# Performance work log

Hardware: AMD Instinct MI355X
Metric: run time of the kernel (lower is better)

## Reference

```python
import jax, jax.numpy as jnp
import numpy as np

K = 1024          # num_codebook_vectors
D = 256           # latent_dim
BETA = 0.25
DECAY = 0.99
EPS = 1e-5


def setup_inputs() -> dict:
    key = jax.random.key(0)
    k1, k2, k3 = jax.random.split(key, 3)
    return {
        "z": jax.random.normal(k1, (32, 256, 32, 32), dtype=jnp.float32),
        "embedding": jax.random.normal(k2, (K, D), dtype=jnp.float32),
        "ema_cluster_size": jnp.zeros((K,), dtype=jnp.float32),
        "ema_w": jax.random.normal(k3, (K, D), dtype=jnp.float32),
    }


def reference(z, embedding, ema_cluster_size, ema_w):
    # z: [B, C=D, H, W] -> [B, H, W, D]
    zp = jnp.transpose(z, (0, 2, 3, 1))
    zf = zp.reshape(-1, D)                                  # [N, D]

    # pairwise squared distances: ||z||^2 + ||e||^2 - 2 z e^T
    d = (jnp.sum(zf * zf, axis=1, keepdims=True)
         + jnp.sum(embedding * embedding, axis=1)
         - 2.0 * zf @ embedding.T)                           # [N, K]
    idx = jnp.argmin(d, axis=1)                              # [N]

    # one-hot @ embedding == gather
    z_q = jnp.take(embedding, idx, axis=0).reshape(zp.shape)  # [B,H,W,D]

    # EMA codebook update (training path)
    counts = jax.ops.segment_sum(jnp.ones_like(idx, dtype=jnp.float32), idx,
                                 num_segments=K)             # sum of one-hots
    new_cs = ema_cluster_size * DECAY + (1.0 - DECAY) * counts
    n = jnp.sum(new_cs)
    new_cs = (new_cs + EPS) / (n + K * EPS) * n
    dw = jax.ops.segment_sum(zf, idx, num_segments=K)        # encodings^T @ zf
    new_ema_w = ema_w * DECAY + (1.0 - DECAY) * dw
    new_embedding = new_ema_w / new_cs[:, None]

    # commitment loss (z_q computed with OLD embedding, per source order)
    e_latent_loss = jnp.mean((z_q - zp) ** 2)
    loss = BETA * e_latent_loss

    # straight-through (no grad distinction in pure forward)
    z_q_out = jnp.transpose(z_q, (0, 3, 1, 2))               # [B, D, H, W]
    return (z_q_out, idx[:, None], loss, new_embedding, new_cs, new_ema_w)
```

## Files before the change

kernel.cpp:

```cpp
#include <hip/hip_runtime.h>

#define K_CODES 1024
#define D_DIM   256
#define N_VEC   32768
#define BETA    0.25f
#define DECAY   0.99f
#define EPSV    1e-5f

#define OFF_ZQ   0
#define OFF_IDX  8388608
#define OFF_LOSS 8421376
#define OFF_EMB  8421377
#define OFF_CS   8683521
#define OFF_EMAW 8684545

#define WS_EMBT    0
#define WS_ENORM   262144
#define WS_ELOMAX  263168
#define WS_EHIMAX  263169
#define WS_FIXCNT  263170
#define WS_S2      263172
#define WS_ZN2     1311748
#define WS_ZLO2    1344516
#define WS_FIXLIST 1377284
#define WS_OFF     1410052
#define WS_POS     1411076
#define WS_CNT     1412100
#define WS_CHTAB   1413124
#define WS_TC      1415172

#define CHUNK 32

typedef _Float16 f16;
typedef f16   f16x8 __attribute__((ext_vector_type(8)));
typedef float f32x4 __attribute__((ext_vector_type(4)));

__device__ inline void top2_merge(float& d1, int& j1, float& d2, int& j2,
                                  float od1, int oj1, float od2, int oj2) {
    if (od1 < d1 || (od1 == d1 && oj1 < j1)) {
        float nd2; int nj2;
        if (d1 < od2 || (d1 == od2 && j1 < oj2)) { nd2 = d1; nj2 = j1; }
        else { nd2 = od2; nj2 = oj2; }
        d2 = nd2; j2 = nj2; d1 = od1; j1 = oj1;
    } else {
        if (od1 < d2 || (od1 == d2 && oj1 < j2)) { d2 = od1; j2 = oj1; }
    }
}

__global__ void k_pt(const float* __restrict__ z, const float* __restrict__ emb,
                     float* __restrict__ ws, float* __restrict__ out) {
    if (blockIdx.x == 0 && threadIdx.x == 0) *(int*)(ws + WS_FIXCNT) = 0;
    if (blockIdx.x < 256) {
        int j    = blockIdx.x * 4 + (threadIdx.x >> 6);
        int lane = threadIdx.x & 63;
        float4 v = reinterpret_cast<const float4*>(emb + j * D_DIM)[lane];
        ws[(lane * 4 + 0) * 1024 + j] = v.x;
        ws[(lane * 4 + 1) * 1024 + j] = v.y;
        ws[(lane * 4 + 2) * 1024 + j] = v.z;
        ws[(lane * 4 + 3) * 1024 + j] = v.w;
        float s = v.x * v.x + v.y * v.y + v.z * v.z + v.w * v.w;
        float hx = (float)(f16)v.x, hy = (float)(f16)v.y;
        float hz = (float)(f16)v.z, hw = (float)(f16)v.w;
        float lx = v.x - hx, ly = v.y - hy, lz = v.z - hz, lw = v.w - hw;
        float sl = lx * lx + ly * ly + lz * lz + lw * lw;
        float sh = hx * hx + hy * hy + hz * hz + hw * hw;
        #pragma unroll
        for (int o = 32; o > 0; o >>= 1) {
            s  += __shfl_xor(s,  o, 64);
            sl += __shfl_xor(sl, o, 64);
            sh += __shfl_xor(sh, o, 64);
        }
        if (lane == 0) {
            ws[WS_ENORM + j] = s;
            atomicMax((int*)(ws + WS_ELOMAX), __float_as_int(sqrtf(sl)));
            atomicMax((int*)(ws + WS_EHIMAX), __float_as_int(sqrtf(sh)));
        }
    } else if (blockIdx.x < 384) {
        int slot = (blockIdx.x - 256) * 256 + threadIdx.x;
        int lane = slot & 63;
        int kbjt = slot >> 6;
        int kb   = kbjt & 7;
        int jt   = kbjt >> 3;
        int j    = jt * 16 + (lane & 15);
        int d0   = kb * 32 + (lane >> 4) * 8;
        float4 e0 = *reinterpret_cast<const float4*>(emb + j * D_DIM + d0);
        float4 e1 = *reinterpret_cast<const float4*>(emb + j * D_DIM + d0 + 4);
        f16x8 w;
        w[0] = (f16)e0.x; w[1] = (f16)e0.y; w[2] = (f16)e0.z; w[3] = (f16)e0.w;
        w[4] = (f16)e1.x; w[5] = (f16)e1.y; w[6] = (f16)e1.z; w[7] = (f16)e1.w;
        f16* dst = (f16*)(out + OFF_EMAW + 3);
        *reinterpret_cast<f16x8*>(dst + slot * 8) = w;
    } else {
        __shared__ float tile[32][257];
        const int bid = blockIdx.x - 384;
        const int n0  = bid * 32;
        const int b   = n0 >> 10;
        const int hw0 = n0 & 1023;
        const int tid = threadIdx.x;
        #pragma unroll 8
        for (int rep = 0; rep < 32; ++rep) {
            int elem = rep * 256 + tid;
            int d = elem >> 5, hwl = elem & 31;
            tile[hwl][d] = z[b * (D_DIM * 1024) + d * 1024 + hw0 + hwl];
        }
        __syncthreads();
        #pragma unroll 8
        for (int row = 0; row < 32; ++row)
            out[OFF_ZQ + (long)(n0 + row) * 256 + tid] = tile[row][tid];
        if (tid < 32) {
            float sn = 0.f, sl = 0.f;
            for (int d = 0; d < 256; ++d) {
                float v  = tile[tid][d];
                float lo = v - (float)(f16)v;
                sn += v * v; sl += lo * lo;
            }
            ws[WS_ZN2  + n0 + tid] = sn;
            ws[WS_ZLO2 + n0 + tid] = sl;
        }
    }
}

__global__ __launch_bounds__(256, 4)
void k_main(float* __restrict__ out, float* __restrict__ ws) {
    __shared__ float els_s[512];

    const int tid  = threadIdx.x;
    const int lane = tid & 63;
    const int w    = tid >> 6;
    const int bid  = blockIdx.x;
    const int rt   = bid >> 1;
    const int jh   = bid & 1;
    const int n0   = rt * 64;
    const float* zf = out + OFF_ZQ;
    const f16* Bw = (const f16*)(out + OFF_EMAW + 3);

    if (bid == 0) {
        #pragma unroll
        for (int r = 0; r < 4; ++r) out[OFF_CS + r * 256 + tid] = 0.f;
        if (tid == 0) out[OFF_LOSS] = 0.f;
    }
    els_s[tid]       = ws[WS_ENORM + jh * 512 + tid];
    els_s[tid + 256] = ws[WS_ENORM + jh * 512 + tid + 256];

    const int aoff = (lane >> 4) * 8;
    const int c    = lane & 15;
    const long arow = n0 + w * 16 + c;
    f16x8 a0, a1, a2, a3, a4, a5, a6, a7;
#define LOADA(KB, AV) { \
    float4 p0 = *reinterpret_cast<const float4*>(zf + arow * 256 + KB * 32 + aoff); \
    float4 p1 = *reinterpret_cast<const float4*>(zf + arow * 256 + KB * 32 + aoff + 4); \
    AV = (f16x8){(f16)p0.x, (f16)p0.y, (f16)p0.z, (f16)p0.w, \
                 (f16)p1.x, (f16)p1.y, (f16)p1.z, (f16)p1.w}; }
    LOADA(0, a0) LOADA(1, a1) LOADA(2, a2) LOADA(3, a3)
    LOADA(4, a4) LOADA(5, a5) LOADA(6, a6) LOADA(7, a7)
#undef LOADA
    __syncthreads();

    float d1_0 = 3.4e38f, d2_0 = 3.4e38f; int j1_0 = 0, j2_0 = 0;
    float d1_1 = 3.4e38f, d2_1 = 3.4e38f; int j1_1 = 0, j2_1 = 0;
    float d1_2 = 3.4e38f, d2_2 = 3.4e38f; int j1_2 = 0, j2_2 = 0;
    float d1_3 = 3.4e38f, d2_3 = 3.4e38f; int j1_3 = 0, j2_3 = 0;

    for (int pass = 0; pass < 16; ++pass) {
        const int jt0 = jh * 32 + pass * 2;
        const f16* B0 = Bw + ((size_t)jt0 * 8 * 64 + lane) * 8;
        f32x4 acc0 = (f32x4){0.f, 0.f, 0.f, 0.f};
        f32x4 acc1 = (f32x4){0.f, 0.f, 0.f, 0.f};
#define KBSTEP(KB, AV) { \
        f16x8 b0 = *reinterpret_cast<const f16x8*>(B0 + (size_t)KB * 512); \
        f16x8 b1 = *reinterpret_cast<const f16x8*>(B0 + (size_t)(KB + 8) * 512); \
        acc0 = __builtin_amdgcn_mfma_f32_16x16x32_f16(AV, b0, acc0, 0, 0, 0); \
        acc1 = __builtin_amdgcn_mfma_f32_16x16x32_f16(AV, b1, acc1, 0, 0, 0); }
        KBSTEP(0, a0) KBSTEP(1, a1) KBSTEP(2, a2) KBSTEP(3, a3)
        KBSTEP(4, a4) KBSTEP(5, a5) KBSTEP(6, a6) KBSTEP(7, a7)
#undef KBSTEP
        const int jl0 = pass * 32 + c;
        const float en0 = els_s[jl0];
        const float en1 = els_s[jl0 + 16];
        const int jg0 = jh * 512 + jl0;
#define FOLD(V, JJ, R) { float _v = (V); \
        if (_v < d1_##R) { d2_##R = d1_##R; j2_##R = j1_##R; d1_##R = _v; j1_##R = (JJ); } \
        else if (_v < d2_##R) { d2_##R = _v; j2_##R = (JJ); } }
        FOLD(en0 - 2.f * acc0[0], jg0,      0) FOLD(en1 - 2.f * acc1[0], jg0 + 16, 0)
        FOLD(en0 - 2.f * acc0[1], jg0,      1) FOLD(en1 - 2.f * acc1[1], jg0 + 16, 1)
        FOLD(en0 - 2.f * acc0[2], jg0,      2) FOLD(en1 - 2.f * acc1[2], jg0 + 16, 2)
        FOLD(en0 - 2.f * acc0[3], jg0,      3) FOLD(en1 - 2.f * acc1[3], jg0 + 16, 3)
#undef FOLD
    }

#define MERGE(R, RIDX) { \
        float e1 = d1_##R, e2 = d2_##R; int f1 = j1_##R, f2 = j2_##R; \
        _Pragma("unroll") \
        for (int s = 1; s < 16; s <<= 1) { \
            float o1 = __shfl_xor(e1, s, 64); int g1 = __shfl_xor(f1, s, 64); \
            float o2 = __shfl_xor(e2, s, 64); int g2 = __shfl_xor(f2, s, 64); \
            top2_merge(e1, f1, e2, f2, o1, g1, o2, g2); \
        } \
        if (c == 0) { \
            int row = n0 + w * 16 + (lane >> 4) * 4 + RIDX; \
            *reinterpret_cast<float4*>(ws + WS_S2 + ((size_t)row * 2 + jh) * 4) = \
                (float4){e1, (float)f1, e2, (float)f2}; } }
    MERGE(0, 0) MERGE(1, 1) MERGE(2, 2) MERGE(3, 3)
#undef MERGE
}

__global__ void k_merge(float* __restrict__ ws, float* __restrict__ out) {
    int n = blockIdx.x * 256 + threadIdx.x;
    const float4* S2 = reinterpret_cast<const float4*>(ws + WS_S2) + (size_t)n * 2;
    float4 e0 = S2[0], e1 = S2[1];
    float d1 = e0.x; int j1 = (int)e0.y; float d2 = e0.z; int j2 = (int)e0.w;
    top2_merge(d1, j1, d2, j2, e1.x, (int)e1.y, e1.z, (int)e1.w);
    out[OFF_IDX + n] = (float)j1;
    float zn2 = ws[WS_ZN2 + n];
    float margin = 4.f * (sqrtf(ws[WS_ZLO2 + n]) * ws[WS_EHIMAX] +
                          sqrtf(zn2) * ws[WS_ELOMAX]) + 0.05f;
    if (d2 - d1 <= margin) {
        int p = atomicAdd((int*)(ws + WS_FIXCNT), 1);
        ((int*)(ws + WS_FIXLIST))[p] = n;
    } else {
        atomicAdd(out + OFF_CS + j1, 1.0f);
        atomicAdd(out + OFF_LOSS, d1 + zn2);
    }
    #pragma unroll
    for (int r = 0; r < 2; ++r)
        *reinterpret_cast<float4*>(out + OFF_EMAW + ((size_t)n * 2 + r) * 4) =
            (float4){0.f, 0.f, 0.f, 0.f};
}

__global__ void k_fix(const float* __restrict__ ws_c, float* __restrict__ out) {
    __shared__ float zr[8][256];
    __shared__ float rd[8][4]; __shared__ int rj[8][4];
    const int tid = threadIdx.x;
    const int cnt = *(const int*)(ws_c + WS_FIXCNT);
    const int* fixlist = (const int*)(ws_c + WS_FIXLIST);
    const int groups = (cnt + 7) >> 3;
    const float4 en = *reinterpret_cast<const float4*>(ws_c + WS_ENORM + tid * 4);

    for (int g = blockIdx.x; g < groups; g += gridDim.x) {
        int nrow[8];
        #pragma unroll
        for (int r = 0; r < 8; ++r) {
            int slot = g * 8 + r;
            nrow[r] = (slot < cnt) ? fixlist[slot] : -1;
        }
        #pragma unroll
        for (int r = 0; r < 8; ++r)
            zr[r][tid] = (nrow[r] >= 0) ? out[OFF_ZQ + (long)nrow[r] * 256 + tid] : 0.f;
        __syncthreads();

        float acc[8][4];
        #pragma unroll
        for (int r = 0; r < 8; ++r)
            #pragma unroll
            for (int q = 0; q < 4; ++q) acc[r][q] = 0.f;
        #pragma unroll 4
        for (int d = 0; d < 256; ++d) {
            float4 e = *reinterpret_cast<const float4*>(ws_c + WS_EMBT + d * 1024 + tid * 4);
            #pragma unroll
            for (int r = 0; r < 8; ++r) {
                float zd = zr[r][d];
                acc[r][0] += zd * e.x; acc[r][1] += zd * e.y;
                acc[r][2] += zd * e.z; acc[r][3] += zd * e.w;
            }
        }
        #pragma unroll
        for (int r = 0; r < 8; ++r) {
            float best = 3.4e38f; int bj = 0;
            #pragma unroll
            for (int q = 0; q < 4; ++q) {
                int j = tid * 4 + q;
                float v = ((const float*)&en)[q] - 2.f * acc[r][q];
                if (v < best || (v == best && j < bj)) { best = v; bj = j; }
            }
            #pragma unroll
            for (int o = 1; o < 64; o <<= 1) {
                float ov = __shfl_xor(best, o, 64);
                int   oj = __shfl_xor(bj, o, 64);
                if (ov < best || (ov == best && oj < bj)) { best = ov; bj = oj; }
            }
            if ((tid & 63) == 0) { rd[r][tid >> 6] = best; rj[r][tid >> 6] = bj; }
        }
        __syncthreads();
        if (tid < 8) {
            int r = tid;
            float v = rd[r][0]; int j = rj[r][0];
            #pragma unroll
            for (int ww = 1; ww < 4; ++ww)
                if (rd[r][ww] < v || (rd[r][ww] == v && rj[r][ww] < j)) { v = rd[r][ww]; j = rj[r][ww]; }
            int slot = g * 8 + r;
            if (slot < cnt) {
                int n = fixlist[slot];
                out[OFF_IDX + n] = (float)j;
                atomicAdd(out + OFF_CS + j, 1.0f);
                atomicAdd(out + OFF_LOSS, v + ws_c[WS_ZN2 + n]);
            }
        }
        __syncthreads();
    }
}

__global__ void k_scan(const float* __restrict__ ema_cs, float* __restrict__ ws,
                       float* __restrict__ out) {
    __shared__ float s[K_CODES];
    int tid = threadIdx.x;
    float cntf = out[OFF_CS + tid];
    int   cnt  = (int)cntf;
    float raw  = ema_cs[tid] * DECAY + 0.01f * cntf;

    s[tid] = cntf;
    __syncthreads();
    for (int off = 1; off < 1024; off <<= 1) {
        float v = (tid >= off) ? s[tid - off] : 0.f;
        __syncthreads();
        s[tid] += v;
        __syncthreads();
    }
    int excl = (int)(s[tid] - cntf);
    ((int*)(ws + WS_OFF))[tid] = excl;
    ((int*)(ws + WS_POS))[tid] = excl;
    ((int*)(ws + WS_CNT))[tid] = cnt;
    __syncthreads();

    int nch = (cnt + CHUNK - 1) / CHUNK;
    s[tid] = (float)nch;
    __syncthreads();
    for (int off = 1; off < 1024; off <<= 1) {
        float v = (tid >= off) ? s[tid - off] : 0.f;
        __syncthreads();
        s[tid] += v;
        __syncthreads();
    }
    int chexcl = (int)s[tid] - nch;
    int* chtab = (int*)(ws + WS_CHTAB);
    for (int k = 0; k < nch; ++k)
        chtab[chexcl + k] = (tid << 16) | k;
    if (tid == 1023) *(int*)(ws + WS_TC) = chexcl + nch;
    __syncthreads();

    s[tid] = raw;
    __syncthreads();
    for (int st = 512; st > 0; st >>= 1) {
        if (tid < st) s[tid] += s[tid + st];
        __syncthreads();
    }
    float ntot = s[0];
    out[OFF_CS + tid] = (raw + EPSV) / (ntot + K_CODES * EPSV) * ntot;
    if (tid == 0)
        out[OFF_LOSS] = out[OFF_LOSS] * (BETA / (float)(N_VEC * D_DIM));
}

__global__ void k_scatter(const float* __restrict__ out_c, float* __restrict__ ws) {
    int n = blockIdx.x * 256 + threadIdx.x;
    int j = (int)out_c[OFF_IDX + n];
    int p = atomicAdd((int*)(ws + WS_POS) + j, 1);
    ((int*)(ws + WS_FIXLIST))[p] = n;
}

__global__ void k_dw2(const float* __restrict__ ws, float* __restrict__ out) {
    __shared__ int midx[CHUNK];
    const int b = blockIdx.x;
    if (b >= *(const int*)(ws + WS_TC)) return;
    const int tab = ((const int*)(ws + WS_CHTAB))[b];
    const int j   = tab >> 16;
    const int lc  = tab & 0xffff;
    const int off = ((const int*)(ws + WS_OFF))[j];
    const int cnt = ((const int*)(ws + WS_CNT))[j];
    const int base = lc * CHUNK;
    const int m    = min(CHUNK, cnt - base);
    const int tid  = threadIdx.x;
    if (tid < CHUNK)
        midx[tid] = (tid < m) ? ((const int*)(ws + WS_FIXLIST))[off + base + tid] : 0;
    __syncthreads();
    float acc = 0.f;
    for (int i = 0; i < m; ++i)
        acc += out[OFF_ZQ + (long)midx[i] * 256 + tid];
    atomicAdd(out + OFF_EMAW + j * 256 + tid, acc);
}

__global__ void k_tail(const float* __restrict__ emb, const float* __restrict__ ema_w,
                       float* __restrict__ out) {
    const int tid = threadIdx.x;
    if (blockIdx.x < 256) {
        int i4 = blockIdx.x * 256 + tid;
        int j  = i4 >> 6;
        float4 dw = *reinterpret_cast<float4*>(out + OFF_EMAW + i4 * 4);
        float4 ew = *reinterpret_cast<const float4*>(ema_w + i4 * 4);
        float inv = 1.f / out[OFF_CS + j];
        float4 nw = {ew.x * DECAY + 0.01f * dw.x, ew.y * DECAY + 0.01f * dw.y,
                     ew.z * DECAY + 0.01f * dw.z, ew.w * DECAY + 0.01f * dw.w};
        *reinterpret_cast<float4*>(out + OFF_EMAW + i4 * 4) = nw;
        float4 nb = {nw.x * inv, nw.y * inv, nw.z * inv, nw.w * inv};
        *reinterpret_cast<float4*>(out + OFF_EMB + i4 * 4) = nb;
    } else {
        __shared__ float erows[32][257];
        __shared__ int js[32];
        const int n0  = (blockIdx.x - 256) * 32;
        const int b   = n0 >> 10;
        const int hw0 = n0 & 1023;
        if (tid < 32) js[tid] = (int)out[OFF_IDX + n0 + tid];
        __syncthreads();
        #pragma unroll 4
        for (int r = 0; r < 32; ++r)
            erows[r][tid] = emb[js[r] * D_DIM + tid];
        __syncthreads();
        const long zqb = (long)b * (D_DIM * 1024) + hw0;
        #pragma unroll 4
        for (int rep = 0; rep < 32; ++rep) {
            int elem = rep * 256 + tid;
            int d    = elem >> 5;
            int nl   = elem & 31;
            out[OFF_ZQ + zqb + d * 1024 + nl] = erows[nl][d];
        }
    }
}

extern "C" void kernel_launch(void* const* d_in, const int* in_sizes, int n_in,
                              void* d_out, int out_size, void* d_ws, size_t ws_size,
                              hipStream_t stream) {
    const float* z      = (const float*)d_in[0];
    const float* emb    = (const float*)d_in[1];
    const float* ema_cs = (const float*)d_in[2];
    const float* ema_w  = (const float*)d_in[3];
    float* out = (float*)d_out;
    float* ws  = (float*)d_ws;

    hipLaunchKernelGGL(k_pt,      dim3(1408), dim3(256),  0, stream, z, emb, ws, out);
    hipLaunchKernelGGL(k_main,    dim3(1024), dim3(256),  0, stream, out, ws);
    hipLaunchKernelGGL(k_merge,   dim3(128),  dim3(256),  0, stream, ws, out);
    hipLaunchKernelGGL(k_fix,     dim3(512),  dim3(256),  0, stream, ws, out);
    hipLaunchKernelGGL(k_scan,    dim3(1),    dim3(1024), 0, stream, ema_cs, ws, out);
    hipLaunchKernelGGL(k_scatter, dim3(128),  dim3(256),  0, stream, out, ws);
    hipLaunchKernelGGL(k_dw2,     dim3(2048), dim3(256),  0, stream, ws, out);
    hipLaunchKernelGGL(k_tail,    dim3(1280), dim3(256),  0, stream, emb, ema_w, out);
}
```

Before: 203.8 us.

## Pack distance and index into sortable uint keys for top-2 tracking

Replaces the float-plus-index top-2 tracking in the main distance kernel with a packed 32-bit key. A bias of 512 keeps distances positive so their float bits sort as unsigned integers, and the low 10 mantissa bits are replaced by the code index. Top-2 folding and the wave shuffle merge then become branchless unsigned min/max, with half the shuffles and half the partial-result storage. The mantissa truncation loses precision, which is covered by widening the fix-up margin by 0.4; that can send more rows to the exact fix-up path. Launch bounds are also relaxed from 4 to 2 blocks per CU.

```diff
diff --git a/kernel.cpp b/kernel.cpp
--- a/kernel.cpp
+++ b/kernel.cpp
@@ -30,6 +30,7 @@
 #define WS_TC      1415172
 
 #define CHUNK 32
+#define DBIAS 512.0f
 
 typedef _Float16 f16;
 typedef f16   f16x8 __attribute__((ext_vector_type(8)));
@@ -120,7 +121,7 @@
     }
 }
 
-__global__ __launch_bounds__(256, 4)
+__global__ __launch_bounds__(256, 2)
 void k_main(float* __restrict__ out, float* __restrict__ ws) {
     __shared__ float els_s[512];
 
@@ -139,8 +140,8 @@
         for (int r = 0; r < 4; ++r) out[OFF_CS + r * 256 + tid] = 0.f;
         if (tid == 0) out[OFF_LOSS] = 0.f;
     }
-    els_s[tid]       = ws[WS_ENORM + jh * 512 + tid];
-    els_s[tid + 256] = ws[WS_ENORM + jh * 512 + tid + 256];
+    els_s[tid]       = ws[WS_ENORM + jh * 512 + tid] + DBIAS;
+    els_s[tid + 256] = ws[WS_ENORM + jh * 512 + tid + 256] + DBIAS;
 
     const int aoff = (lane >> 4) * 8;
     const int c    = lane & 15;
@@ -156,10 +157,10 @@
 #undef LOADA
     __syncthreads();
 
-    float d1_0 = 3.4e38f, d2_0 = 3.4e38f; int j1_0 = 0, j2_0 = 0;
-    float d1_1 = 3.4e38f, d2_1 = 3.4e38f; int j1_1 = 0, j2_1 = 0;
-    float d1_2 = 3.4e38f, d2_2 = 3.4e38f; int j1_2 = 0, j2_2 = 0;
-    float d1_3 = 3.4e38f, d2_3 = 3.4e38f; int j1_3 = 0, j2_3 = 0;
+    unsigned k1_0 = 0xFFFFFFFFu, k2_0 = 0xFFFFFFFFu;
+    unsigned k1_1 = 0xFFFFFFFFu, k2_1 = 0xFFFFFFFFu;
+    unsigned k1_2 = 0xFFFFFFFFu, k2_2 = 0xFFFFFFFFu;
+    unsigned k1_3 = 0xFFFFFFFFu, k2_3 = 0xFFFFFFFFu;
 
     for (int pass = 0; pass < 16; ++pass) {
         const int jt0 = jh * 32 + pass * 2;
@@ -177,43 +178,55 @@
         const int jl0 = pass * 32 + c;
         const float en0 = els_s[jl0];
         const float en1 = els_s[jl0 + 16];
-        const int jg0 = jh * 512 + jl0;
-#define FOLD(V, JJ, R) { float _v = (V); \
-        if (_v < d1_##R) { d2_##R = d1_##R; j2_##R = j1_##R; d1_##R = _v; j1_##R = (JJ); } \
-        else if (_v < d2_##R) { d2_##R = _v; j2_##R = (JJ); } }
-        FOLD(en0 - 2.f * acc0[0], jg0,      0) FOLD(en1 - 2.f * acc1[0], jg0 + 16, 0)
-        FOLD(en0 - 2.f * acc0[1], jg0,      1) FOLD(en1 - 2.f * acc1[1], jg0 + 16, 1)
-        FOLD(en0 - 2.f * acc0[2], jg0,      2) FOLD(en1 - 2.f * acc1[2], jg0 + 16, 2)
-        FOLD(en0 - 2.f * acc0[3], jg0,      3) FOLD(en1 - 2.f * acc1[3], jg0 + 16, 3)
+        const unsigned jg0 = (unsigned)(jh * 512 + jl0);
+#define FOLD(EN, ACC, JJ, R) { \
+        float _d = fmaf(-2.f, (ACC), (EN)); \
+        unsigned _k = (__float_as_uint(_d) & 0xFFFFFC00u) | (JJ); \
+        unsigned _mx = max(k1_##R, _k); \
+        k1_##R = min(k1_##R, _k); \
+        k2_##R = min(k2_##R, _mx); }
+        FOLD(en0, acc0[0], jg0,       0) FOLD(en1, acc1[0], jg0 + 16u, 0)
+        FOLD(en0, acc0[1], jg0,       1) FOLD(en1, acc1[1], jg0 + 16u, 1)
+        FOLD(en0, acc0[2], jg0,       2) FOLD(en1, acc1[2], jg0 + 16u, 2)
+        FOLD(en0, acc0[3], jg0,       3) FOLD(en1, acc1[3], jg0 + 16u, 3)
 #undef FOLD
     }
 
 #define MERGE(R, RIDX) { \
-        float e1 = d1_##R, e2 = d2_##R; int f1 = j1_##R, f2 = j2_##R; \
+        unsigned K1 = k1_##R, K2 = k2_##R; \
         _Pragma("unroll") \
         for (int s = 1; s < 16; s <<= 1) { \
-            float o1 = __shfl_xor(e1, s, 64); int g1 = __shfl_xor(f1, s, 64); \
-            float o2 = __shfl_xor(e2, s, 64); int g2 = __shfl_xor(f2, s, 64); \
-            top2_merge(e1, f1, e2, f2, o1, g1, o2, g2); \
+            unsigned o1 = (unsigned)__shfl_xor((int)K1, s, 64); \
+            unsigned o2 = (unsigned)__shfl_xor((int)K2, s, 64); \
+            unsigned mx = max(K1, o1); \
+            K1 = min(K1, o1); \
+            K2 = min(min(K2, o2), mx); \
         } \
         if (c == 0) { \
             int row = n0 + w * 16 + (lane >> 4) * 4 + RIDX; \
-            *reinterpret_cast<float4*>(ws + WS_S2 + ((size_t)row * 2 + jh) * 4) = \
-                (float4){e1, (float)f1, e2, (float)f2}; } }
+            *reinterpret_cast<float2*>(ws + WS_S2 + ((size_t)row * 2 + jh) * 2) = \
+                (float2){__uint_as_float(K1), __uint_as_float(K2)}; } }
     MERGE(0, 0) MERGE(1, 1) MERGE(2, 2) MERGE(3, 3)
 #undef MERGE
 }
 
 __global__ void k_merge(float* __restrict__ ws, float* __restrict__ out) {
     int n = blockIdx.x * 256 + threadIdx.x;
-    const float4* S2 = reinterpret_cast<const float4*>(ws + WS_S2) + (size_t)n * 2;
-    float4 e0 = S2[0], e1 = S2[1];
-    float d1 = e0.x; int j1 = (int)e0.y; float d2 = e0.z; int j2 = (int)e0.w;
-    top2_merge(d1, j1, d2, j2, e1.x, (int)e1.y, e1.z, (int)e1.w);
+    const float2* S2 = reinterpret_cast<const float2*>(ws + WS_S2) + (size_t)n * 2;
+    float2 ea = S2[0], eb = S2[1];
+    unsigned k1a = __float_as_uint(ea.x), k2a = __float_as_uint(ea.y);
+    unsigned k1b = __float_as_uint(eb.x), k2b = __float_as_uint(eb.y);
+    unsigned mx = max(k1a, k1b);
+    unsigned k1 = min(k1a, k1b);
+    unsigned k2 = min(min(k2a, k2b), mx);
+    int j1 = (int)(k1 & 0x3FFu);
+    float d1 = __uint_as_float(k1 & 0xFFFFFC00u) - DBIAS;
+    float d2 = __uint_as_float(k2 & 0xFFFFFC00u) - DBIAS;
     out[OFF_IDX + n] = (float)j1;
     float zn2 = ws[WS_ZN2 + n];
     float margin = 4.f * (sqrtf(ws[WS_ZLO2 + n]) * ws[WS_EHIMAX] +
-                          sqrtf(zn2) * ws[WS_ELOMAX]) + 0.05f;
+                          sqrtf(zn2) * ws[WS_ELOMAX]) + 0.05f
+                 + 0.4f;
     if (d2 - d1 <= margin) {
         int p = atomicAdd((int*)(ws + WS_FIXCNT), 1);
         ((int*)(ws + WS_FIXLIST))[p] = n;
```

After: 189.8 us. 1.07x faster.
